# Optimization experiments

Measured on AMD Instinct MI355X. Metric: run time of the kernel, lower is better.

Reference implementation:

```python
import jax, jax.numpy as jnp
import numpy as np

B, C, H, W = 8, 64, 256, 256  # dim=64 -> chunks 32/16/8/8

def _dwconv3x3(x, w, b):
    # x: [N,Cg,H,W], w: [Cg,1,3,3] depthwise
    y = jax.lax.conv_general_dilated(
        x, w, window_strides=(1, 1), padding=((1, 1), (1, 1)),
        feature_group_count=x.shape[1],
        dimension_numbers=('NCHW', 'OIHW', 'NCHW'))
    return y + b[None, :, None, None]

def _maxpool4(x):
    # exact 4x4/stride-4 max pool == adaptive_max_pool2d when sizes divide
    return jax.lax.reduce_window(x, -jnp.inf, jax.lax.max,
                                 (1, 1, 4, 4), (1, 1, 4, 4), 'VALID')

def _upnearest(x, s):
    # nearest interpolate to (H,W) from (H/s,W/s) == repeat by s
    return jnp.repeat(jnp.repeat(x, s, axis=2), s, axis=3)

def setup_inputs() -> dict:
    key = jax.random.key(0)
    ks = jax.random.split(key, 11)
    sc = 0.05
    return {
        'x':  jax.random.normal(ks[0], (B, C, H, W), jnp.float32),
        'w1': jax.random.normal(ks[1], (32, 1, 3, 3), jnp.float32) * sc,
        'b1': jax.random.normal(ks[2], (32,), jnp.float32) * sc,
        'w2': jax.random.normal(ks[3], (16, 1, 3, 3), jnp.float32) * sc,
        'b2': jax.random.normal(ks[4], (16,), jnp.float32) * sc,
        'w3': jax.random.normal(ks[5], (8, 1, 3, 3), jnp.float32) * sc,
        'b3': jax.random.normal(ks[6], (8,), jnp.float32) * sc,
        'w4': jax.random.normal(ks[7], (8, 1, 3, 3), jnp.float32) * sc,
        'b4': jax.random.normal(ks[8], (8,), jnp.float32) * sc,
        'wa': jax.random.normal(ks[9], (64, 64), jnp.float32) * sc,  # 1x1 conv
        'ba': jax.random.normal(ks[10], (64,), jnp.float32) * sc,
    }

def reference(x, w1, b1, w2, b2, w3, b3, w4, b4, wa, ba):
    c = x.shape[1]
    xa, xb = x[:, : c // 2], x[:, c // 2 :]            # 32 / 32 channels
    x1 = _dwconv3x3(xa, w1, b1)                        # [B,32,H,W]
    p2 = _maxpool4(xb)                                 # [B,32,H/4,W/4]
    p2a, p2b = p2[:, :16], p2[:, 16:]
    x2 = _upnearest(_dwconv3x3(p2a, w2, b2), 4)        # [B,16,H,W]
    p3 = _maxpool4(p2b)                                # [B,16,H/16,W/16]
    p3a, p3b = p3[:, :8], p3[:, 8:]
    x3 = _upnearest(_dwconv3x3(p3a, w3, b3), 16)       # [B,8,H,W]
    p4 = _maxpool4(p3b)                                # [B,8,H/64,W/64]
    x4 = _upnearest(_dwconv3x3(p4, w4, b4), 64)        # [B,8,H,W]
    cat = jnp.concatenate([x1, x2, x3, x4], axis=1)    # [B,64,H,W]
    agg = jnp.einsum('oc,bchw->bohw', wa, cat) + ba[None, :, None, None]
    return jax.nn.gelu(agg, approximate=False) * x
```

## Files before the change

### kernel.cpp

```cpp
#include <hip/hip_runtime.h>
#include <math.h>

#define NB 8
#define NC 64
#define NH 256
#define NW 256

typedef short short8 __attribute__((ext_vector_type(8)));
typedef float f32x4 __attribute__((ext_vector_type(4)));

__device__ __forceinline__ unsigned short f2bf(float f) {
    unsigned int u = __float_as_uint(f);
    u += 0x7FFFu + ((u >> 16) & 1u);
    return (unsigned short)(u >> 16);
}

__device__ __forceinline__ int slot_of(int px, int g) {
    return g ^ (px & 7) ^ ((px >> 3) & 7);
}

__launch_bounds__(1024)
__global__ void pyramid_kernel(const float* __restrict__ x,
                               const float* __restrict__ w2, const float* __restrict__ b2,
                               const float* __restrict__ w3, const float* __restrict__ b3,
                               const float* __restrict__ w4, const float* __restrict__ b4,
                               float* __restrict__ x2c, float* __restrict__ x3c,
                               float* __restrict__ x4c) {
    __shared__ float pl[64 * 65];
    __shared__ float pl2[16 * 17];
    __shared__ float pl3[16];

    const int tid = threadIdx.x;
    const int c = blockIdx.x & 31;
    const int b = blockIdx.x >> 5;
    const size_t plane = (size_t)NH * NW;
    const float* src = x + ((size_t)(b * 64 + 32 + c)) * plane;

#pragma unroll
    for (int i = 0; i < 4; ++i) {
        int o = tid + 1024 * i;
        int pw = o & 63, ph = o >> 6;
        const float* s2 = src + (size_t)(ph * 4) * NW + pw * 4;
        float m = -INFINITY;
#pragma unroll
        for (int r = 0; r < 4; ++r) {
            float4 v = *reinterpret_cast<const float4*>(s2 + (size_t)r * NW);
            m = fmaxf(m, fmaxf(fmaxf(v.x, v.y), fmaxf(v.z, v.w)));
        }
        pl[ph * 65 + pw] = m;
    }
    __syncthreads();

    if (c < 16) {
        float* dst = x2c + ((size_t)(b * 16 + c)) * 4096;
        const float* wc = w2 + c * 9;
        float bb = b2[c];
#pragma unroll
        for (int i = 0; i < 4; ++i) {
            int o = tid + 1024 * i;
            int pw = o & 63, ph = o >> 6;
            float acc = bb;
#pragma unroll
            for (int dy = -1; dy <= 1; ++dy) {
                int yy = ph + dy;
                if (yy < 0 || yy >= 64) continue;
#pragma unroll
                for (int dx = -1; dx <= 1; ++dx) {
                    int xx = pw + dx;
                    if (xx < 0 || xx >= 64) continue;
                    acc += pl[yy * 65 + xx] * wc[(dy + 1) * 3 + (dx + 1)];
                }
            }
            dst[o] = acc;
        }
    } else {
        if (tid < 256) {
            int pw = tid & 15, ph = tid >> 4;
            float m = -INFINITY;
#pragma unroll
            for (int r = 0; r < 4; ++r)
#pragma unroll
                for (int cc = 0; cc < 4; ++cc)
                    m = fmaxf(m, pl[(ph * 4 + r) * 65 + pw * 4 + cc]);
            pl2[ph * 17 + pw] = m;
        }
        __syncthreads();
        if (c < 24) {
            if (tid < 256) {
                int pw = tid & 15, ph = tid >> 4;
                const float* wc = w3 + (c - 16) * 9;
                float acc = b3[c - 16];
#pragma unroll
                for (int dy = -1; dy <= 1; ++dy) {
                    int yy = ph + dy;
                    if (yy < 0 || yy >= 16) continue;
#pragma unroll
                    for (int dx = -1; dx <= 1; ++dx) {
                        int xx = pw + dx;
                        if (xx < 0 || xx >= 16) continue;
                        acc += pl2[yy * 17 + xx] * wc[(dy + 1) * 3 + (dx + 1)];
                    }
                }
                x3c[((size_t)(b * 8 + (c - 16))) * 256 + tid] = acc;
            }
        } else {
            if (tid < 16) {
                int pw = tid & 3, ph = tid >> 2;
                float m = -INFINITY;
#pragma unroll
                for (int r = 0; r < 4; ++r)
#pragma unroll
                    for (int cc = 0; cc < 4; ++cc)
                        m = fmaxf(m, pl2[(ph * 4 + r) * 17 + pw * 4 + cc]);
                pl3[ph * 4 + pw] = m;
            }
            __syncthreads();
            if (tid < 16) {
                int pw = tid & 3, ph = tid >> 2;
                const float* wc = w4 + (c - 24) * 9;
                float acc = b4[c - 24];
#pragma unroll
                for (int dy = -1; dy <= 1; ++dy) {
                    int yy = ph + dy;
                    if (yy < 0 || yy >= 4) continue;
#pragma unroll
                    for (int dx = -1; dx <= 1; ++dx) {
                        int xx = pw + dx;
                        if (xx < 0 || xx >= 4) continue;
                        acc += pl3[yy * 4 + xx] * wc[(dy + 1) * 3 + (dx + 1)];
                    }
                }
                x4c[((size_t)(b * 8 + (c - 24))) * 16 + tid] = acc;
            }
        }
    }
}

__launch_bounds__(256)
__global__ void fused_main(const float* __restrict__ x,
                           const float* __restrict__ w1, const float* __restrict__ b1,
                           const float* __restrict__ x2c,
                           const float* __restrict__ x3c,
                           const float* __restrict__ x4c,
                           const float* __restrict__ wa, const float* __restrict__ ba,
                           float* __restrict__ out) {
    __shared__ __align__(16) unsigned short cat_lds[256 * 64];
    __shared__ __align__(16) unsigned short wa_lds[64 * 64];

    const int tid = threadIdx.x;
    const int q = tid & 63;
    const int cg = tid >> 6;
    const int blk = blockIdx.x;
    const int b = blk & 7;
    const int h = blk >> 3;
    const size_t plane = (size_t)NH * NW;
    const float* xb = x + (size_t)b * NC * plane;

    {
        int r = tid >> 2;
        int g0 = (tid & 3) * 2;
#pragma unroll
        for (int gg = 0; gg < 2; ++gg) {
            int g = g0 + gg;
            const float* srcw = wa + r * 64 + g * 8;
            int4 pk;
            pk.x = (unsigned)f2bf(srcw[0]) | ((unsigned)f2bf(srcw[1]) << 16);
            pk.y = (unsigned)f2bf(srcw[2]) | ((unsigned)f2bf(srcw[3]) << 16);
            pk.z = (unsigned)f2bf(srcw[4]) | ((unsigned)f2bf(srcw[5]) << 16);
            pk.w = (unsigned)f2bf(srcw[6]) | ((unsigned)f2bf(srcw[7]) << 16);
            *reinterpret_cast<int4*>(&wa_lds[r * 64 + slot_of(r, g) * 8]) = pk;
        }
    }

    float pv[8];
    {
        const int h4 = h >> 2, h16 = h >> 4, h64 = h >> 6;
        if (cg == 0) {
#pragma unroll
            for (int j = 0; j < 8; ++j)
                pv[j] = x2c[(((size_t)b * 16 + j) * 64 + h4) * 64 + q];
        } else if (cg == 1) {
#pragma unroll
            for (int j = 0; j < 8; ++j)
                pv[j] = x2c[(((size_t)b * 16 + 8 + j) * 64 + h4) * 64 + q];
        } else if (cg == 2) {
#pragma unroll
            for (int j = 0; j < 8; ++j)
                pv[j] = x3c[(((size_t)b * 8 + j) * 16 + h16) * 16 + (q >> 2)];
        } else {
#pragma unroll
            for (int j = 0; j < 8; ++j)
                pv[j] = x4c[(((size_t)b * 8 + j) * 4 + h64) * 4 + (q >> 4)];
        }
    }

    const bool hv0 = (h > 0), hv2 = (h < NH - 1);
    const int hm = hv0 ? h - 1 : h;
    const int hp = hv2 ? h + 1 : h;
    float conv[8][4];
#pragma unroll
    for (int j = 0; j < 8; ++j) {
        const int c = cg * 8 + j;
        const float* srcc = xb + (size_t)c * plane;
        float4 a0 = *reinterpret_cast<const float4*>(srcc + (size_t)hm * NW + 4 * q);
        float4 a1 = *reinterpret_cast<const float4*>(srcc + (size_t)h  * NW + 4 * q);
        float4 a2 = *reinterpret_cast<const float4*>(srcc + (size_t)hp * NW + 4 * q);
        const float* wc = w1 + c * 9;
        float k0 = hv0 ? wc[0] : 0.f, k1 = hv0 ? wc[1] : 0.f, k2 = hv0 ? wc[2] : 0.f;
        float k3 = wc[3], k4 = wc[4], k5 = wc[5];
        float k6 = hv2 ? wc[6] : 0.f, k7 = hv2 ? wc[7] : 0.f, k8 = hv2 ? wc[8] : 0.f;
        float p0 = __shfl_up(a0.w, 1), p1 = __shfl_up(a1.w, 1), p2 = __shfl_up(a2.w, 1);
        float n0 = __shfl_down(a0.x, 1), n1 = __shfl_down(a1.x, 1), n2 = __shfl_down(a2.x, 1);
        if (q == 0)  { p0 = 0.f; p1 = 0.f; p2 = 0.f; }
        if (q == 63) { n0 = 0.f; n1 = 0.f; n2 = 0.f; }
        float r0[6] = {p0, a0.x, a0.y, a0.z, a0.w, n0};
        float r1[6] = {p1, a1.x, a1.y, a1.z, a1.w, n1};
        float r2[6] = {p2, a2.x, a2.y, a2.z, a2.w, n2};
#pragma unroll
        for (int i = 0; i < 4; ++i) {
            conv[j][i] = k0 * r0[i] + k1 * r0[i + 1] + k2 * r0[i + 2]
                       + k3 * r1[i] + k4 * r1[i + 1] + k5 * r1[i + 2]
                       + k6 * r2[i] + k7 * r2[i + 1] + k8 * r2[i + 2]
                       + b1[c];
        }
    }
#pragma unroll
    for (int i = 0; i < 4; ++i) {
        int px = 4 * q + i;
        int4 pk;
        pk.x = (unsigned)f2bf(conv[0][i]) | ((unsigned)f2bf(conv[1][i]) << 16);
        pk.y = (unsigned)f2bf(conv[2][i]) | ((unsigned)f2bf(conv[3][i]) << 16);
        pk.z = (unsigned)f2bf(conv[4][i]) | ((unsigned)f2bf(conv[5][i]) << 16);
        pk.w = (unsigned)f2bf(conv[6][i]) | ((unsigned)f2bf(conv[7][i]) << 16);
        *reinterpret_cast<int4*>(&cat_lds[px * 64 + slot_of(px, cg) * 8]) = pk;
    }
    {
        int4 pk;
        pk.x = (unsigned)f2bf(pv[0]) | ((unsigned)f2bf(pv[1]) << 16);
        pk.y = (unsigned)f2bf(pv[2]) | ((unsigned)f2bf(pv[3]) << 16);
        pk.z = (unsigned)f2bf(pv[4]) | ((unsigned)f2bf(pv[5]) << 16);
        pk.w = (unsigned)f2bf(pv[6]) | ((unsigned)f2bf(pv[7]) << 16);
#pragma unroll
        for (int i = 0; i < 4; ++i) {
            int px = 4 * q + i;
            *reinterpret_cast<int4*>(&cat_lds[px * 64 + slot_of(px, 4 + cg) * 8]) = pk;
        }
    }

    __syncthreads();

    const int lane = tid & 63;
    const int lr = lane & 15;
    const int lk = lane >> 4;
    const int pxb = cg * 64;

    short8 bfrag[4][2];
#pragma unroll
    for (int nt = 0; nt < 4; ++nt) {
        int px = pxb + nt * 16 + lr;
#pragma unroll
        for (int kt = 0; kt < 2; ++kt) {
            int g = kt * 4 + lk;
            bfrag[nt][kt] = *reinterpret_cast<const short8*>(
                &cat_lds[px * 64 + slot_of(px, g) * 8]);
        }
    }
    __syncthreads();

    const size_t outrow = (size_t)h * NW;
    size_t goff[4];
#pragma unroll
    for (int i = 0; i < 4; ++i)
        goff[i] = ((size_t)(b * 64 + cg + 4 * i)) * plane + outrow + q * 4;

    float4 xcur[4], xnxt[4];
#pragma unroll
    for (int i = 0; i < 4; ++i)
        xcur[i] = *reinterpret_cast<const float4*>(&x[goff[i]]);

#pragma unroll
    for (int mt = 0; mt < 4; ++mt) {
        short8 afrag[2];
        int row = mt * 16 + lr;
#pragma unroll
        for (int kt = 0; kt < 2; ++kt) {
            int g = kt * 4 + lk;
            afrag[kt] = *reinterpret_cast<const short8*>(
                &wa_lds[row * 64 + slot_of(row, g) * 8]);
        }
        int obase = mt * 16 + lk * 4;
        float bs0 = ba[obase], bs1 = ba[obase + 1], bs2 = ba[obase + 2], bs3 = ba[obase + 3];
        f32x4 acc[4];
#pragma unroll
        for (int nt = 0; nt < 4; ++nt) {
            acc[nt][0] = bs0; acc[nt][1] = bs1; acc[nt][2] = bs2; acc[nt][3] = bs3;
        }
#pragma unroll
        for (int nt = 0; nt < 4; ++nt)
#pragma unroll
            for (int kt = 0; kt < 2; ++kt)
                acc[nt] = __builtin_amdgcn_mfma_f32_16x16x32_bf16(
                    afrag[kt], bfrag[nt][kt], acc[nt], 0, 0, 0);

        float* buf = reinterpret_cast<float*>(cat_lds) + (mt & 1) * 4096;
#pragma unroll
        for (int nt = 0; nt < 4; ++nt) {
            int px = pxb + nt * 16 + lr;
#pragma unroll
            for (int r = 0; r < 4; ++r) {
                int rw = lk * 4 + r;
                float a = acc[nt][r];
                float gl = 0.5f * a * (1.0f + erff(a * 0.70710678118654752f));
                buf[rw * 256 + (px ^ ((rw & 7) << 2))] = gl;
            }
        }
        __syncthreads();

        if (mt < 3) {
#pragma unroll
            for (int i = 0; i < 4; ++i)
                xnxt[i] = *reinterpret_cast<const float4*>(
                    &x[goff[i] + (size_t)((mt + 1) * 16) * plane]);
        }

#pragma unroll
        for (int i = 0; i < 4; ++i) {
            int chLoc = cg + 4 * i;
            float4 gv = *reinterpret_cast<const float4*>(
                &buf[chLoc * 256 + ((q * 4) ^ ((chLoc & 7) << 2))]);
            size_t off = goff[i] + (size_t)(mt * 16) * plane;
            float4 ov;
            ov.x = gv.x * xcur[i].x; ov.y = gv.y * xcur[i].y;
            ov.z = gv.z * xcur[i].z; ov.w = gv.w * xcur[i].w;
            *reinterpret_cast<float4*>(&out[off]) = ov;
        }
#pragma unroll
        for (int i = 0; i < 4; ++i) xcur[i] = xnxt[i];
    }
}

extern "C" void kernel_launch(void* const* d_in, const int* in_sizes, int n_in,
                              void* d_out, int out_size, void* d_ws, size_t ws_size,
                              hipStream_t stream) {
    const float* x  = (const float*)d_in[0];
    const float* w1 = (const float*)d_in[1];
    const float* b1 = (const float*)d_in[2];
    const float* w2 = (const float*)d_in[3];
    const float* b2 = (const float*)d_in[4];
    const float* w3 = (const float*)d_in[5];
    const float* b3 = (const float*)d_in[6];
    const float* w4 = (const float*)d_in[7];
    const float* b4 = (const float*)d_in[8];
    const float* wa = (const float*)d_in[9];
    const float* ba = (const float*)d_in[10];
    float* out = (float*)d_out;

    float* ws  = (float*)d_ws;
    float* x2c = ws;
    float* x3c = x2c + 524288;
    float* x4c = x3c + 16384;

    pyramid_kernel<<<NB * 32, 1024, 0, stream>>>(x, w2, b2, w3, b3, w4, b4,
                                                 x2c, x3c, x4c);
    fused_main<<<NB * NH, 256, 0, stream>>>(x, w1, b1, x2c, x3c, x4c, wa, ba, out);
}
```

Baseline: 282.5 us.

## Write GELU output directly from MFMA accumulators and use tanh-approx GELU

Drops the LDS round-trip used to transpose the MFMA accumulator tile into float4 rows, along with the per-tile barriers. Each lane now loads its matching x elements and stores gelu(acc)*x straight to global memory, prefetching the next tile's x. Exact erf GELU is replaced by a sigmoid/tanh-style approximation built on __expf and a hardware reciprocal. The global accesses become scalar 16-lane-contiguous loads and stores instead of float4, and the approximation changes numerics compared with the exact erf GELU.

```diff
diff --git a/kernel.cpp b/kernel.cpp
--- a/kernel.cpp
+++ b/kernel.cpp
@@ -13,6 +13,13 @@
     unsigned int u = __float_as_uint(f);
     u += 0x7FFFu + ((u >> 16) & 1u);
     return (unsigned short)(u >> 16);
+}
+
+__device__ __forceinline__ float fast_gelu(float a) {
+    float s = a * a;
+    float z = a * fmaf(s, 0.0713548f, 1.5957691f);
+    float e = __expf(-z);
+    return a * __builtin_amdgcn_rcpf(1.0f + e);
 }
 
 __device__ __forceinline__ int slot_of(int px, int g) {
@@ -247,12 +254,22 @@
         }
     }
 
-    __syncthreads();
-
     const int lane = tid & 63;
     const int lr = lane & 15;
     const int lk = lane >> 4;
     const int pxb = cg * 64;
+    const size_t gbase = (size_t)(b * 64 + lk * 4) * plane + (size_t)h * NW + pxb + lr;
+    const float* xg_p = x + gbase;
+    float* og_p = out + gbase;
+
+    float xg[4][4], xn[4][4];
+#pragma unroll
+    for (int nt = 0; nt < 4; ++nt)
+#pragma unroll
+        for (int r = 0; r < 4; ++r)
+            xg[nt][r] = xg_p[(size_t)r * plane + nt * 16];
+
+    __syncthreads();
 
     short8 bfrag[4][2];
 #pragma unroll
@@ -265,18 +282,6 @@
                 &cat_lds[px * 64 + slot_of(px, g) * 8]);
         }
     }
-    __syncthreads();
-
-    const size_t outrow = (size_t)h * NW;
-    size_t goff[4];
-#pragma unroll
-    for (int i = 0; i < 4; ++i)
-        goff[i] = ((size_t)(b * 64 + cg + 4 * i)) * plane + outrow + q * 4;
-
-    float4 xcur[4], xnxt[4];
-#pragma unroll
-    for (int i = 0; i < 4; ++i)
-        xcur[i] = *reinterpret_cast<const float4*>(&x[goff[i]]);
 
 #pragma unroll
     for (int mt = 0; mt < 4; ++mt) {
@@ -302,40 +307,26 @@
                 acc[nt] = __builtin_amdgcn_mfma_f32_16x16x32_bf16(
                     afrag[kt], bfrag[nt][kt], acc[nt], 0, 0, 0);
 
-        float* buf = reinterpret_cast<float*>(cat_lds) + (mt & 1) * 4096;
-#pragma unroll
-        for (int nt = 0; nt < 4; ++nt) {
-            int px = pxb + nt * 16 + lr;
+        if (mt < 3) {
+#pragma unroll
+            for (int nt = 0; nt < 4; ++nt)
+#pragma unroll
+                for (int r = 0; r < 4; ++r)
+                    xn[nt][r] = xg_p[(size_t)((mt + 1) * 16 + r) * plane + nt * 16];
+        }
+
+#pragma unroll
+        for (int nt = 0; nt < 4; ++nt)
 #pragma unroll
             for (int r = 0; r < 4; ++r) {
-                int rw = lk * 4 + r;
-                float a = acc[nt][r];
-                float gl = 0.5f * a * (1.0f + erff(a * 0.70710678118654752f));
-                buf[rw * 256 + (px ^ ((rw & 7) << 2))] = gl;
-            }
-        }
-        __syncthreads();
-
-        if (mt < 3) {
-#pragma unroll
-            for (int i = 0; i < 4; ++i)
-                xnxt[i] = *reinterpret_cast<const float4*>(
-                    &x[goff[i] + (size_t)((mt + 1) * 16) * plane]);
-        }
-
-#pragma unroll
-        for (int i = 0; i < 4; ++i) {
-            int chLoc = cg + 4 * i;
-            float4 gv = *reinterpret_cast<const float4*>(
-                &buf[chLoc * 256 + ((q * 4) ^ ((chLoc & 7) << 2))]);
-            size_t off = goff[i] + (size_t)(mt * 16) * plane;
-            float4 ov;
-            ov.x = gv.x * xcur[i].x; ov.y = gv.y * xcur[i].y;
-            ov.z = gv.z * xcur[i].z; ov.w = gv.w * xcur[i].w;
-            *reinterpret_cast<float4*>(&out[off]) = ov;
-        }
-#pragma unroll
-        for (int i = 0; i < 4; ++i) xcur[i] = xnxt[i];
+                float gl = fast_gelu(acc[nt][r]);
+                og_p[(size_t)(mt * 16 + r) * plane + nt * 16] = gl * xg[nt][r];
+            }
+#pragma unroll
+        for (int nt = 0; nt < 4; ++nt)
+#pragma unroll
+            for (int r = 0; r < 4; ++r)
+                xg[nt][r] = xn[nt][r];
     }
 }
 
```

New measurement: 297.2 us. +5.2%, slower.
